# Performance work log

Hardware: AMD Instinct MI355X
Metric: run time of the kernel (lower is better)

## Reference

```python
import jax, jax.numpy as jnp
import numpy as np

B, S, D = 2, 2048, 1024
H, DQK = 16, 64          # n_head, d_qk = d_O // n_head
DV = 64                  # d_v = d_O // n_head
TEMP = DQK ** 0.5
EPS = 1e-6


def relu15(x):
    # ReLU capped at 15 (custom non-softmax attention activation)
    return jnp.clip(x, 0.0, 15.0)


def setup_inputs() -> dict:
    key = jax.random.key(0)
    ks = jax.random.split(key, 10)
    s = 0.02
    return {
        "q": jax.random.normal(ks[0], (B, S, D), jnp.float32),
        "k": jax.random.normal(ks[1], (B, S, D), jnp.float32),
        "v": jax.random.normal(ks[2], (B, S, D), jnp.float32),
        "Wq": jax.random.normal(ks[3], (D, H * DQK), jnp.float32) * s,
        "Wk": jax.random.normal(ks[4], (D, H * DQK), jnp.float32) * s,
        "Wv": jax.random.normal(ks[5], (D, H * DV), jnp.float32) * s,
        "Wfc": jax.random.normal(ks[6], (H * DV, H * DV), jnp.float32) * s,
        "gamma": jnp.ones((H * DV,), jnp.float32),
        "beta": jnp.zeros((H * DV,), jnp.float32),
    }


def reference(q, k, v, Wq, Wk, Wv, Wfc, gamma, beta):
    residual = q                                   # d_Q == d_O path
    # QKV projections (no bias)
    qh = (q @ Wq).reshape(B, S, H, DQK).transpose(0, 2, 1, 3)   # [B,H,S,dqk]
    kh = (k @ Wk).reshape(B, S, H, DQK).transpose(0, 2, 1, 3)
    vh = (v @ Wv).reshape(B, S, H, DV).transpose(0, 2, 1, 3)
    # custom attention: scaled scores -> ReLU15 (no softmax normalization)
    attn = jnp.einsum('bhqd,bhkd->bhqk', qh / TEMP, kh)          # [B,H,S,S]
    attn = relu15(attn)
    o = jnp.einsum('bhqk,bhkd->bhqd', attn, vh)                  # [B,H,S,dv]
    o = o.transpose(0, 2, 1, 3).reshape(B, S, H * DV)            # [B,S,d_O]
    # output projection + residual + LayerNorm
    o = o @ Wfc + residual
    mu = jnp.mean(o, axis=-1, keepdims=True)
    var = jnp.var(o, axis=-1, keepdims=True)
    o = (o - mu) / jnp.sqrt(var + EPS) * gamma + beta
    return o
```

## Files before the change

kernel.cpp:

```cpp
#include <hip/hip_runtime.h>
#include <stdint.h>

#define DEV static __device__ __forceinline__

typedef __attribute__((ext_vector_type(4)))  float f32x4;
typedef __attribute__((ext_vector_type(16))) float f32x16;
typedef __bf16 bf16x8 __attribute__((ext_vector_type(8)));

constexpr int Bc = 2, S = 2048, Dm = 1024, H = 16, DH = 64;
constexpr int BS  = Bc * S;
constexpr int HSZ = Bc * H * S * DH;

constexpr size_t OFF_QKVB  = 0;
constexpr size_t OFF_WT    = 25165824;
constexpr size_t OFF_HEADS = 33554432;
constexpr size_t OFF_VT    = 58720256;
constexpr size_t OFF_O     = 67108864;

DEV uint16_t f2bf(float f) {
    uint32_t u = __float_as_uint(f);
    uint32_t r = u + 0x7FFFu + ((u >> 16) & 1u);
    return (uint16_t)(r >> 16);
}
DEV uint32_t pk2bf(float lo, float hi) {
    return (uint32_t)f2bf(lo) | ((uint32_t)f2bf(hi) << 16);
}
DEV uint32_t swz128(uint32_t byteoff) {
    return byteoff ^ (((byteoff >> 7) & 7u) << 4);
}
DEV void gll16(const void* g, void* l) {
    auto gp = (const __attribute__((address_space(1))) uint32_t*)g;
    auto lp = (__attribute__((address_space(3))) uint32_t*)l;
    __builtin_amdgcn_global_load_lds(gp, lp, 16, 0, 0);
}
DEV bf16x8 ld_frag(const char* base, uint32_t logical_off) {
    return __builtin_bit_cast(bf16x8, *(const uint4*)(base + swz128(logical_off)));
}
DEV bf16x8 ld_frag_g(const void* p) {
    return __builtin_bit_cast(bf16x8, *(const uint4*)p);
}

__global__ __launch_bounds__(256) void k_convert(const float* __restrict__ q,
                                                 const float* __restrict__ k,
                                                 const float* __restrict__ v,
                                                 uint16_t* __restrict__ out) {
    const int64_t n1 = (int64_t)BS * Dm;
    int64_t i = ((int64_t)blockIdx.x * 256 + threadIdx.x) * 8;
    const float* src; int64_t j;
    if (i < n1)            { src = q; j = i; }
    else if (i < 2 * n1)   { src = k; j = i - n1; }
    else                   { src = v; j = i - 2 * n1; }
    float4 a = *(const float4*)(src + j);
    float4 b = *(const float4*)(src + j + 4);
    union { uint16_t u[8]; uint4 q4; } o;
    o.u[0] = f2bf(a.x); o.u[1] = f2bf(a.y); o.u[2] = f2bf(a.z); o.u[3] = f2bf(a.w);
    o.u[4] = f2bf(b.x); o.u[5] = f2bf(b.y); o.u[6] = f2bf(b.z); o.u[7] = f2bf(b.w);
    *(uint4*)(out + i) = o.q4;
}

__global__ __launch_bounds__(256) void k_transw(const float* __restrict__ w0,
                                                const float* __restrict__ w1,
                                                const float* __restrict__ w2,
                                                const float* __restrict__ w3,
                                                uint16_t* __restrict__ wt) {
    int mat = blockIdx.y;
    const float* w = (mat == 0) ? w0 : (mat == 1) ? w1 : (mat == 2) ? w2 : w3;
    float scale = (mat == 0) ? 0.125f : 1.0f;
    uint16_t* out = wt + (size_t)mat * 1024 * 1024;
    int tile = blockIdx.x;
    int tr = (tile >> 4) << 6, tc = (tile & 15) << 6;
    __shared__ float lds[64][65];
    int t = threadIdx.x;
#pragma unroll
    for (int p = 0; p < 4; ++p) {
        int r = p * 16 + (t >> 4);
        int c = (t & 15) * 4;
        float4 x = *(const float4*)(w + (size_t)(tr + r) * 1024 + tc + c);
        lds[r][c] = x.x; lds[r][c + 1] = x.y; lds[r][c + 2] = x.z; lds[r][c + 3] = x.w;
    }
    __syncthreads();
    int n = t >> 2, kc = (t & 3) * 16;
    union { uint16_t u[16]; uint4 q[2]; } tt;
#pragma unroll
    for (int j = 0; j < 16; ++j) tt.u[j] = f2bf(lds[kc + j][n] * scale);
    uint16_t* dst = out + (size_t)(tc + n) * 1024 + tr + kc;
    *(uint4*)dst = tt.q[0];
    *(uint4*)(dst + 8) = tt.q[1];
}

struct Acc { f32x4 a[4][4]; };

DEV void stage128(const uint16_t* g, int ldbytes, char* lds) {
    int tid = threadIdx.x;
#pragma unroll
    for (int it = 0; it < 4; ++it) {
        uint32_t p = it * 4096 + tid * 16;
        uint32_t lo = swz128(p);
        uint32_t row = lo >> 7, col = lo & 127;
        gll16((const char*)g + (size_t)row * ldbytes + col,
              lds + it * 4096 + (tid & ~63) * 16);
    }
}

DEV void gemm_core(const uint16_t* A, const uint16_t* Bt, int K,
                   char* la, char* lb, Acc& acc) {
    int lane = threadIdx.x & 63, w = threadIdx.x >> 6;
    int wr = w >> 1, wc = w & 1;
#pragma unroll
    for (int mf = 0; mf < 4; ++mf)
#pragma unroll
        for (int nf = 0; nf < 4; ++nf)
#pragma unroll
            for (int r = 0; r < 4; ++r) acc.a[mf][nf][r] = 0.f;
    for (int k0 = 0; k0 < K; k0 += 64) {
        __syncthreads();
        stage128(A + k0, K * 2, la);
        stage128(Bt + k0, K * 2, lb);
        __syncthreads();
#pragma unroll
        for (int kk = 0; kk < 2; ++kk) {
            bf16x8 af[4], bfr[4];
#pragma unroll
            for (int mf = 0; mf < 4; ++mf) {
                uint32_t row = wr * 64 + mf * 16 + (lane & 15);
                af[mf] = ld_frag(la, row * 128 + kk * 64 + (lane >> 4) * 16);
            }
#pragma unroll
            for (int nf = 0; nf < 4; ++nf) {
                uint32_t row = wc * 64 + nf * 16 + (lane & 15);
                bfr[nf] = ld_frag(lb, row * 128 + kk * 64 + (lane >> 4) * 16);
            }
#pragma unroll
            for (int mf = 0; mf < 4; ++mf)
#pragma unroll
                for (int nf = 0; nf < 4; ++nf)
                    acc.a[mf][nf] = __builtin_amdgcn_mfma_f32_16x16x32_bf16(
                        af[mf], bfr[nf], acc.a[mf][nf], 0, 0, 0);
        }
    }
}

__global__ __launch_bounds__(256) void k_proj(const uint16_t* __restrict__ qkvb,
                                              const uint16_t* __restrict__ WT,
                                              uint16_t* __restrict__ heads) {
    __shared__ char lds[32768];
    int blk = blockIdx.x;
    int sel = blk >> 8;
    int t2 = blk & 255; int bm = t2 >> 3, bn = t2 & 7;
    const uint16_t* A  = qkvb + (size_t)sel * BS * Dm + (size_t)bm * 128 * Dm;
    const uint16_t* Bt = WT   + (size_t)sel * Dm * Dm + (size_t)bn * 128 * Dm;
    Acc acc;
    gemm_core(A, Bt, 1024, lds, lds + 16384, acc);
    uint16_t* out = heads + (size_t)sel * HSZ;
    int lane = threadIdx.x & 63, w = threadIdx.x >> 6;
    int m_base = bm * 128 + (w >> 1) * 64, n_base = bn * 128 + (w & 1) * 64;
#pragma unroll
    for (int mf = 0; mf < 4; ++mf)
#pragma unroll
        for (int nf = 0; nf < 4; ++nf)
#pragma unroll
            for (int r = 0; r < 4; ++r) {
                int m = m_base + mf * 16 + (lane >> 4) * 4 + r;
                int n = n_base + nf * 16 + (lane & 15);
                int b = m >> 11, s = m & 2047, h = n >> 6, d = n & 63;
                out[(((size_t)(b * H + h)) * S + s) * 64 + d] = f2bf(acc.a[mf][nf][r]);
            }
}

__global__ __launch_bounds__(256) void k_transv(const uint16_t* __restrict__ Vh,
                                                uint16_t* __restrict__ Vt) {
    int bh = blockIdx.x >> 5, st = blockIdx.x & 31;
    int s0 = st * 64;
    const uint16_t* src = Vh + (size_t)bh * S * 64 + (size_t)s0 * 64;
    uint16_t* dst = Vt + (size_t)bh * 64 * S;
    __shared__ uint16_t lds[64][65];
    int t = threadIdx.x;
    {
        int r = t >> 2, c = (t & 3) * 16;
        union { uint16_t u[16]; uint4 q[2]; } x;
        x.q[0] = *(const uint4*)(src + (size_t)r * 64 + c);
        x.q[1] = *(const uint4*)(src + (size_t)r * 64 + c + 8);
#pragma unroll
        for (int j = 0; j < 16; ++j) lds[r][c + j] = x.u[j];
    }
    __syncthreads();
    {
        int d = t >> 2, sc = (t & 3) * 16;
        union { uint16_t u[16]; uint4 q[2]; } x;
#pragma unroll
        for (int j = 0; j < 16; ++j) x.u[j] = lds[sc + j][d];
        uint16_t* p = dst + (size_t)d * S + s0 + sc;
        *(uint4*)p = x.q[0];
        *(uint4*)(p + 8) = x.q[1];
    }
}

__global__ __launch_bounds__(512) void k_attn(const uint16_t* __restrict__ Qh,
                                              const uint16_t* __restrict__ Kh,
                                              const uint16_t* __restrict__ Vt,
                                              uint16_t* __restrict__ O) {
    __shared__ char kbuf[2][8192];
    __shared__ char vbuf[2][8192];
    int bh = blockIdx.x >> 3, qb = (blockIdx.x & 7) * 256;
    int tid = threadIdx.x, lane = tid & 63, w = tid >> 6;
    int l31 = lane & 31, hi = lane >> 5;
    const char* Kbase = (const char*)(Kh + (size_t)bh * S * 64);
    const char* Vbase = (const char*)(Vt + (size_t)bh * 64 * S);

    bf16x8 qf[4];
    {
        const char* qrow = (const char*)(Qh + (size_t)bh * S * 64
                                         + (size_t)(qb + w * 32 + l31) * 64);
#pragma unroll
        for (int ks = 0; ks < 4; ++ks)
            qf[ks] = ld_frag_g(qrow + ks * 32 + hi * 16);
    }
    f32x16 oa[2];
#pragma unroll
    for (int nt = 0; nt < 2; ++nt)
#pragma unroll
        for (int r = 0; r < 16; ++r) oa[nt][r] = 0.f;

    auto stageKV = [&](int tile, int bufi) {
        int kv0 = tile * 64;
        uint32_t p = tid * 16;
        uint32_t lo = swz128(p);
        uint32_t row = lo >> 7, col = lo & 127;
        gll16(Kbase + (size_t)(kv0 + row) * 128 + col, kbuf[bufi] + (tid & ~63) * 16);
        gll16(Vbase + (size_t)row * 4096 + (size_t)kv0 * 2 + col, vbuf[bufi] + (tid & ~63) * 16);
    };

    stageKV(0, 0);
    __syncthreads();
    for (int t = 0; t < 32; ++t) {
        int cur = t & 1;
        if (t < 31) stageKV(t + 1, cur ^ 1);
        __builtin_amdgcn_s_setprio(1);
#pragma unroll
        for (int mt = 0; mt < 2; ++mt) {
            f32x16 c;
#pragma unroll
            for (int r = 0; r < 16; ++r) c[r] = 0.f;
#pragma unroll
            for (int ks = 0; ks < 4; ++ks) {
                uint32_t row = mt * 32 + l31;
                bf16x8 a = ld_frag(kbuf[cur], row * 128 + ks * 32 + hi * 16);
                c = __builtin_amdgcn_mfma_f32_32x32x16_bf16(a, qf[ks], c, 0, 0, 0);
            }
#pragma unroll
            for (int r = 0; r < 16; ++r) c[r] = fminf(fmaxf(c[r], 0.f), 15.f);
#pragma unroll
            for (int ks2 = 0; ks2 < 2; ++ks2) {
                uint32_t wds[4];
#pragma unroll
                for (int jj = 0; jj < 2; ++jj) {
                    uint32_t sA = pk2bf(c[8 * ks2 + 2 * jj],     c[8 * ks2 + 2 * jj + 1]);
                    uint32_t sB = pk2bf(c[8 * ks2 + 4 + 2 * jj], c[8 * ks2 + 4 + 2 * jj + 1]);
                    asm volatile("v_permlane32_swap_b32 %0, %1" : "+v"(sA), "+v"(sB));
                    wds[jj] = sA; wds[2 + jj] = sB;
                }
                union { uint32_t w[4]; bf16x8 v; } pa;
                pa.w[0] = wds[0]; pa.w[1] = wds[1]; pa.w[2] = wds[2]; pa.w[3] = wds[3];
#pragma unroll
                for (int nt = 0; nt < 2; ++nt) {
                    uint32_t row = nt * 32 + l31;
                    uint32_t kcol = mt * 64 + ks2 * 32 + hi * 16;
                    bf16x8 vb = ld_frag(vbuf[cur], row * 128 + kcol);
                    oa[nt] = __builtin_amdgcn_mfma_f32_32x32x16_bf16(pa.v, vb, oa[nt], 0, 0, 0);
                }
            }
        }
        __builtin_amdgcn_s_setprio(0);
        __syncthreads();
    }
    int b = bh >> 4, h = bh & 15;
#pragma unroll
    for (int nt = 0; nt < 2; ++nt)
#pragma unroll
        for (int r = 0; r < 16; ++r) {
            int qg = qb + w * 32 + (r & 3) + 8 * (r >> 2) + 4 * hi;
            int col = h * 64 + nt * 32 + l31;
            O[((size_t)(b * S + qg)) * 1024 + col] = f2bf(oa[nt][r]);
        }
}

__global__ __launch_bounds__(256) void k_fc(const uint16_t* __restrict__ Ob,
                                            const uint16_t* __restrict__ WfcT,
                                            const float* __restrict__ resid,
                                            float* __restrict__ out) {
    __shared__ char lds[32768];
    int blk = blockIdx.x;
    int bm = blk >> 3, bn = blk & 7;
    const uint16_t* A  = Ob   + (size_t)bm * 128 * Dm;
    const uint16_t* Bt = WfcT + (size_t)bn * 128 * Dm;
    Acc acc;
    gemm_core(A, Bt, 1024, lds, lds + 16384, acc);
    int lane = threadIdx.x & 63, w = threadIdx.x >> 6;
    int m_base = bm * 128 + (w >> 1) * 64, n_base = bn * 128 + (w & 1) * 64;
#pragma unroll
    for (int mf = 0; mf < 4; ++mf)
#pragma unroll
        for (int nf = 0; nf < 4; ++nf)
#pragma unroll
            for (int r = 0; r < 4; ++r) {
                int m = m_base + mf * 16 + (lane >> 4) * 4 + r;
                int n = n_base + nf * 16 + (lane & 15);
                size_t idx = (size_t)m * 1024 + n;
                out[idx] = acc.a[mf][nf][r] + resid[idx];
            }
}

__global__ __launch_bounds__(256) void k_ln(float* __restrict__ io,
                                            const float* __restrict__ gamma,
                                            const float* __restrict__ beta) {
    int row = blockIdx.x;
    float* p = io + (size_t)row * 1024;
    int t = threadIdx.x;
    float4 x = *(const float4*)(p + t * 4);
    float s  = x.x + x.y + x.z + x.w;
    float s2 = x.x * x.x + x.y * x.y + x.z * x.z + x.w * x.w;
#pragma unroll
    for (int o = 32; o > 0; o >>= 1) { s += __shfl_xor(s, o); s2 += __shfl_xor(s2, o); }
    __shared__ float red[8];
    int w = t >> 6, lane = t & 63;
    if (lane == 0) { red[w] = s; red[4 + w] = s2; }
    __syncthreads();
    s  = red[0] + red[1] + red[2] + red[3];
    s2 = red[4] + red[5] + red[6] + red[7];
    float mu  = s * (1.f / 1024.f);
    float var = s2 * (1.f / 1024.f) - mu * mu;
    float inv = rsqrtf(var + 1e-6f);
    float4 g  = *(const float4*)(gamma + t * 4);
    float4 bb = *(const float4*)(beta + t * 4);
    x.x = (x.x - mu) * inv * g.x + bb.x;
    x.y = (x.y - mu) * inv * g.y + bb.y;
    x.z = (x.z - mu) * inv * g.z + bb.z;
    x.w = (x.w - mu) * inv * g.w + bb.w;
    *(float4*)(p + t * 4) = x;
}

extern "C" void kernel_launch(void* const* d_in, const int* in_sizes, int n_in,
                              void* d_out, int out_size, void* d_ws, size_t ws_size,
                              hipStream_t stream) {
    (void)in_sizes; (void)n_in; (void)out_size; (void)ws_size;
    const float* q     = (const float*)d_in[0];
    const float* k     = (const float*)d_in[1];
    const float* v     = (const float*)d_in[2];
    const float* Wq    = (const float*)d_in[3];
    const float* Wk    = (const float*)d_in[4];
    const float* Wv    = (const float*)d_in[5];
    const float* Wfc   = (const float*)d_in[6];
    const float* gamma = (const float*)d_in[7];
    const float* beta  = (const float*)d_in[8];
    char* ws = (char*)d_ws;
    uint16_t* qkvb  = (uint16_t*)(ws + OFF_QKVB);
    uint16_t* WT    = (uint16_t*)(ws + OFF_WT);
    uint16_t* heads = (uint16_t*)(ws + OFF_HEADS);
    uint16_t* Vt    = (uint16_t*)(ws + OFF_VT);
    uint16_t* Ob    = (uint16_t*)(ws + OFF_O);
    float* out = (float*)d_out;

    k_convert<<<dim3(6144), dim3(256), 0, stream>>>(q, k, v, qkvb);
    k_transw <<<dim3(256, 4), dim3(256), 0, stream>>>(Wq, Wk, Wv, Wfc, WT);
    k_proj   <<<dim3(768), dim3(256), 0, stream>>>(qkvb, WT, heads);
    k_transv <<<dim3(1024), dim3(256), 0, stream>>>(heads + 2 * (size_t)HSZ, Vt);
    k_attn   <<<dim3(256), dim3(512), 0, stream>>>(heads, heads + HSZ, Vt, Ob);
    k_fc     <<<dim3(256), dim3(256), 0, stream>>>(Ob, WT + 3 * 1024 * 1024, q, out);
    k_ln     <<<dim3(4096), dim3(256), 0, stream>>>(out, gamma, beta);
}
```

Measured before the change: 250.2 us.

## Restructure attention to two query tiles per wave and vectorize GEMM epilogues

The attention kernel now uses 128-thread blocks, each wave handling 64 query rows (two 32-row sub-tiles). This reuses K and V LDS fragments across both sub-tiles and doubles MFMA work per load. The projection and FC GEMMs swap operand roles so each lane holds four contiguous output columns, which allows packed bf16 and float4 stores and residual loads. Block indices are remapped across the grid to change cache locality. Hardware v_cvt_pk_bf16_f32 and v_med3 replace the software bf16 rounding and the clamp, which may change rounding behaviour slightly and raises register pressure in attention.

```diff
diff --git a/kernel.cpp b/kernel.cpp
--- a/kernel.cpp
+++ b/kernel.cpp
@@ -22,8 +22,15 @@
     uint32_t r = u + 0x7FFFu + ((u >> 16) & 1u);
     return (uint16_t)(r >> 16);
 }
-DEV uint32_t pk2bf(float lo, float hi) {
-    return (uint32_t)f2bf(lo) | ((uint32_t)f2bf(hi) << 16);
+DEV uint32_t cvtpk(float lo, float hi) {
+    uint32_t r;
+    asm("v_cvt_pk_bf16_f32 %0, %1, %2" : "=v"(r) : "v"(lo), "v"(hi));
+    return r;
+}
+DEV float clip15(float x, float c15) {
+    float r;
+    asm("v_med3_f32 %0, %1, 0, %2" : "=v"(r) : "v"(x), "v"(c15));
+    return r;
 }
 DEV uint32_t swz128(uint32_t byteoff) {
     return byteoff ^ (((byteoff >> 7) & 7u) << 4);
@@ -102,40 +109,40 @@
     }
 }
 
-DEV void gemm_core(const uint16_t* A, const uint16_t* Bt, int K,
+DEV void gemm_core(const uint16_t* Ta, const uint16_t* Tb, int K,
                    char* la, char* lb, Acc& acc) {
     int lane = threadIdx.x & 63, w = threadIdx.x >> 6;
     int wr = w >> 1, wc = w & 1;
 #pragma unroll
-    for (int mf = 0; mf < 4; ++mf)
-#pragma unroll
-        for (int nf = 0; nf < 4; ++nf)
-#pragma unroll
-            for (int r = 0; r < 4; ++r) acc.a[mf][nf][r] = 0.f;
+    for (int ia = 0; ia < 4; ++ia)
+#pragma unroll
+        for (int ib = 0; ib < 4; ++ib)
+#pragma unroll
+            for (int r = 0; r < 4; ++r) acc.a[ia][ib][r] = 0.f;
     for (int k0 = 0; k0 < K; k0 += 64) {
         __syncthreads();
-        stage128(A + k0, K * 2, la);
-        stage128(Bt + k0, K * 2, lb);
+        stage128(Ta + k0, K * 2, la);
+        stage128(Tb + k0, K * 2, lb);
         __syncthreads();
 #pragma unroll
         for (int kk = 0; kk < 2; ++kk) {
             bf16x8 af[4], bfr[4];
 #pragma unroll
-            for (int mf = 0; mf < 4; ++mf) {
-                uint32_t row = wr * 64 + mf * 16 + (lane & 15);
-                af[mf] = ld_frag(la, row * 128 + kk * 64 + (lane >> 4) * 16);
+            for (int ia = 0; ia < 4; ++ia) {
+                uint32_t row = wr * 64 + ia * 16 + (lane & 15);
+                af[ia] = ld_frag(la, row * 128 + kk * 64 + (lane >> 4) * 16);
             }
 #pragma unroll
-            for (int nf = 0; nf < 4; ++nf) {
-                uint32_t row = wc * 64 + nf * 16 + (lane & 15);
-                bfr[nf] = ld_frag(lb, row * 128 + kk * 64 + (lane >> 4) * 16);
+            for (int ib = 0; ib < 4; ++ib) {
+                uint32_t row = wc * 64 + ib * 16 + (lane & 15);
+                bfr[ib] = ld_frag(lb, row * 128 + kk * 64 + (lane >> 4) * 16);
             }
 #pragma unroll
-            for (int mf = 0; mf < 4; ++mf)
-#pragma unroll
-                for (int nf = 0; nf < 4; ++nf)
-                    acc.a[mf][nf] = __builtin_amdgcn_mfma_f32_16x16x32_bf16(
-                        af[mf], bfr[nf], acc.a[mf][nf], 0, 0, 0);
+            for (int ia = 0; ia < 4; ++ia)
+#pragma unroll
+                for (int ib = 0; ib < 4; ++ib)
+                    acc.a[ia][ib] = __builtin_amdgcn_mfma_f32_16x16x32_bf16(
+                        af[ia], bfr[ib], acc.a[ia][ib], 0, 0, 0);
         }
     }
 }
@@ -144,27 +151,29 @@
                                               const uint16_t* __restrict__ WT,
                                               uint16_t* __restrict__ heads) {
     __shared__ char lds[32768];
-    int blk = blockIdx.x;
+    int raw = blockIdx.x;
+    int blk = (raw & 7) * 96 + (raw >> 3);
     int sel = blk >> 8;
     int t2 = blk & 255; int bm = t2 >> 3, bn = t2 & 7;
-    const uint16_t* A  = qkvb + (size_t)sel * BS * Dm + (size_t)bm * 128 * Dm;
-    const uint16_t* Bt = WT   + (size_t)sel * Dm * Dm + (size_t)bn * 128 * Dm;
+    const uint16_t* Act = qkvb + (size_t)sel * BS * Dm + (size_t)bm * 128 * Dm;
+    const uint16_t* Wtt = WT   + (size_t)sel * Dm * Dm + (size_t)bn * 128 * Dm;
     Acc acc;
-    gemm_core(A, Bt, 1024, lds, lds + 16384, acc);
+    gemm_core(Wtt, Act, 1024, lds, lds + 16384, acc);
     uint16_t* out = heads + (size_t)sel * HSZ;
     int lane = threadIdx.x & 63, w = threadIdx.x >> 6;
-    int m_base = bm * 128 + (w >> 1) * 64, n_base = bn * 128 + (w & 1) * 64;
-#pragma unroll
-    for (int mf = 0; mf < 4; ++mf)
-#pragma unroll
-        for (int nf = 0; nf < 4; ++nf)
-#pragma unroll
-            for (int r = 0; r < 4; ++r) {
-                int m = m_base + mf * 16 + (lane >> 4) * 4 + r;
-                int n = n_base + nf * 16 + (lane & 15);
-                int b = m >> 11, s = m & 2047, h = n >> 6, d = n & 63;
-                out[(((size_t)(b * H + h)) * S + s) * 64 + d] = f2bf(acc.a[mf][nf][r]);
-            }
+    int na = bn * 128 + (w >> 1) * 64, mb = bm * 128 + (w & 1) * 64;
+#pragma unroll
+    for (int ia = 0; ia < 4; ++ia)
+#pragma unroll
+        for (int ib = 0; ib < 4; ++ib) {
+            int n0 = na + ia * 16 + (lane >> 4) * 4;
+            int m  = mb + ib * 16 + (lane & 15);
+            uint2 d;
+            d.x = cvtpk(acc.a[ia][ib][0], acc.a[ia][ib][1]);
+            d.y = cvtpk(acc.a[ia][ib][2], acc.a[ia][ib][3]);
+            int b = m >> 11, s = m & 2047, h = n0 >> 6, dd = n0 & 63;
+            *(uint2*)(out + (((size_t)(b * H + h)) * S + s) * 64 + dd) = d;
+        }
 }
 
 __global__ __launch_bounds__(256) void k_transv(const uint16_t* __restrict__ Vh,
@@ -195,39 +204,50 @@
     }
 }
 
-__global__ __launch_bounds__(512) void k_attn(const uint16_t* __restrict__ Qh,
+__global__ __launch_bounds__(128) void k_attn(const uint16_t* __restrict__ Qh,
                                               const uint16_t* __restrict__ Kh,
                                               const uint16_t* __restrict__ Vt,
                                               uint16_t* __restrict__ O) {
     __shared__ char kbuf[2][8192];
     __shared__ char vbuf[2][8192];
-    int bh = blockIdx.x >> 3, qb = (blockIdx.x & 7) * 256;
+    int raw = blockIdx.x;
+    int bid = (raw & 7) * 64 + (raw >> 3);
+    int bh = bid >> 4, qb = (bid & 15) * 128;
     int tid = threadIdx.x, lane = tid & 63, w = tid >> 6;
     int l31 = lane & 31, hi = lane >> 5;
     const char* Kbase = (const char*)(Kh + (size_t)bh * S * 64);
     const char* Vbase = (const char*)(Vt + (size_t)bh * 64 * S);
 
-    bf16x8 qf[4];
-    {
+    bf16x8 qf[2][4];
+#pragma unroll
+    for (int qs = 0; qs < 2; ++qs) {
         const char* qrow = (const char*)(Qh + (size_t)bh * S * 64
-                                         + (size_t)(qb + w * 32 + l31) * 64);
+                                         + (size_t)(qb + w * 64 + qs * 32 + l31) * 64);
 #pragma unroll
         for (int ks = 0; ks < 4; ++ks)
-            qf[ks] = ld_frag_g(qrow + ks * 32 + hi * 16);
-    }
-    f32x16 oa[2];
-#pragma unroll
-    for (int nt = 0; nt < 2; ++nt)
-#pragma unroll
-        for (int r = 0; r < 16; ++r) oa[nt][r] = 0.f;
+            qf[qs][ks] = ld_frag_g(qrow + ks * 32 + hi * 16);
+    }
+    f32x16 oa[2][2];
+#pragma unroll
+    for (int qs = 0; qs < 2; ++qs)
+#pragma unroll
+        for (int nt = 0; nt < 2; ++nt)
+#pragma unroll
+            for (int r = 0; r < 16; ++r) oa[qs][nt][r] = 0.f;
+    float c15 = 15.0f;
 
     auto stageKV = [&](int tile, int bufi) {
         int kv0 = tile * 64;
-        uint32_t p = tid * 16;
-        uint32_t lo = swz128(p);
-        uint32_t row = lo >> 7, col = lo & 127;
-        gll16(Kbase + (size_t)(kv0 + row) * 128 + col, kbuf[bufi] + (tid & ~63) * 16);
-        gll16(Vbase + (size_t)row * 4096 + (size_t)kv0 * 2 + col, vbuf[bufi] + (tid & ~63) * 16);
+#pragma unroll
+        for (int it = 0; it < 4; ++it) {
+            uint32_t p = it * 2048 + tid * 16;
+            uint32_t lo = swz128(p);
+            uint32_t row = lo >> 7, col = lo & 127;
+            gll16(Kbase + (size_t)(kv0 + row) * 128 + col,
+                  kbuf[bufi] + it * 2048 + (tid & ~63) * 16);
+            gll16(Vbase + (size_t)row * 4096 + (size_t)kv0 * 2 + col,
+                  vbuf[bufi] + it * 2048 + (tid & ~63) * 16);
+        }
     };
 
     stageKV(0, 0);
@@ -238,50 +258,64 @@
         __builtin_amdgcn_s_setprio(1);
 #pragma unroll
         for (int mt = 0; mt < 2; ++mt) {
-            f32x16 c;
-#pragma unroll
-            for (int r = 0; r < 16; ++r) c[r] = 0.f;
-#pragma unroll
-            for (int ks = 0; ks < 4; ++ks) {
-                uint32_t row = mt * 32 + l31;
-                bf16x8 a = ld_frag(kbuf[cur], row * 128 + ks * 32 + hi * 16);
-                c = __builtin_amdgcn_mfma_f32_32x32x16_bf16(a, qf[ks], c, 0, 0, 0);
-            }
-#pragma unroll
-            for (int r = 0; r < 16; ++r) c[r] = fminf(fmaxf(c[r], 0.f), 15.f);
-#pragma unroll
-            for (int ks2 = 0; ks2 < 2; ++ks2) {
-                uint32_t wds[4];
-#pragma unroll
-                for (int jj = 0; jj < 2; ++jj) {
-                    uint32_t sA = pk2bf(c[8 * ks2 + 2 * jj],     c[8 * ks2 + 2 * jj + 1]);
-                    uint32_t sB = pk2bf(c[8 * ks2 + 4 + 2 * jj], c[8 * ks2 + 4 + 2 * jj + 1]);
-                    asm volatile("v_permlane32_swap_b32 %0, %1" : "+v"(sA), "+v"(sB));
-                    wds[jj] = sA; wds[2 + jj] = sB;
-                }
-                union { uint32_t w[4]; bf16x8 v; } pa;
-                pa.w[0] = wds[0]; pa.w[1] = wds[1]; pa.w[2] = wds[2]; pa.w[3] = wds[3];
-#pragma unroll
-                for (int nt = 0; nt < 2; ++nt) {
-                    uint32_t row = nt * 32 + l31;
-                    uint32_t kcol = mt * 64 + ks2 * 32 + hi * 16;
-                    bf16x8 vb = ld_frag(vbuf[cur], row * 128 + kcol);
-                    oa[nt] = __builtin_amdgcn_mfma_f32_32x32x16_bf16(pa.v, vb, oa[nt], 0, 0, 0);
+            bf16x8 kf[4];
+#pragma unroll
+            for (int ks = 0; ks < 4; ++ks)
+                kf[ks] = ld_frag(kbuf[cur], (mt * 32 + l31) * 128 + ks * 32 + hi * 16);
+            bf16x8 pa[2][2];
+#pragma unroll
+            for (int qs = 0; qs < 2; ++qs) {
+                f32x16 c;
+#pragma unroll
+                for (int r = 0; r < 16; ++r) c[r] = 0.f;
+#pragma unroll
+                for (int ks = 0; ks < 4; ++ks)
+                    c = __builtin_amdgcn_mfma_f32_32x32x16_bf16(kf[ks], qf[qs][ks], c, 0, 0, 0);
+#pragma unroll
+                for (int r = 0; r < 16; ++r) c[r] = clip15(c[r], c15);
+#pragma unroll
+                for (int ks2 = 0; ks2 < 2; ++ks2) {
+                    union { uint32_t w[4]; bf16x8 v; } up;
+#pragma unroll
+                    for (int jj = 0; jj < 2; ++jj) {
+                        uint32_t sA = cvtpk(c[8 * ks2 + 2 * jj],     c[8 * ks2 + 2 * jj + 1]);
+                        uint32_t sB = cvtpk(c[8 * ks2 + 4 + 2 * jj], c[8 * ks2 + 4 + 2 * jj + 1]);
+                        asm volatile("v_permlane32_swap_b32 %0, %1" : "+v"(sA), "+v"(sB));
+                        up.w[jj] = sA; up.w[2 + jj] = sB;
+                    }
+                    pa[qs][ks2] = up.v;
                 }
             }
+#pragma unroll
+            for (int ks2 = 0; ks2 < 2; ++ks2)
+#pragma unroll
+                for (int nt = 0; nt < 2; ++nt) {
+                    bf16x8 vb = ld_frag(vbuf[cur],
+                                        (nt * 32 + l31) * 128 + mt * 64 + ks2 * 32 + hi * 16);
+#pragma unroll
+                    for (int qs = 0; qs < 2; ++qs)
+                        oa[qs][nt] = __builtin_amdgcn_mfma_f32_32x32x16_bf16(
+                            vb, pa[qs][ks2], oa[qs][nt], 0, 0, 0);
+                }
         }
         __builtin_amdgcn_s_setprio(0);
         __syncthreads();
     }
     int b = bh >> 4, h = bh & 15;
 #pragma unroll
-    for (int nt = 0; nt < 2; ++nt)
-#pragma unroll
-        for (int r = 0; r < 16; ++r) {
-            int qg = qb + w * 32 + (r & 3) + 8 * (r >> 2) + 4 * hi;
-            int col = h * 64 + nt * 32 + l31;
-            O[((size_t)(b * S + qg)) * 1024 + col] = f2bf(oa[nt][r]);
-        }
+    for (int qs = 0; qs < 2; ++qs) {
+        int q = qb + w * 64 + qs * 32 + l31;
+#pragma unroll
+        for (int nt = 0; nt < 2; ++nt)
+#pragma unroll
+            for (int g = 0; g < 4; ++g) {
+                uint2 d;
+                d.x = cvtpk(oa[qs][nt][4 * g],     oa[qs][nt][4 * g + 1]);
+                d.y = cvtpk(oa[qs][nt][4 * g + 2], oa[qs][nt][4 * g + 3]);
+                int col = h * 64 + nt * 32 + 8 * g + 4 * hi;
+                *(uint2*)(O + ((size_t)(b * S + q)) * 1024 + col) = d;
+            }
+    }
 }
 
 __global__ __launch_bounds__(256) void k_fc(const uint16_t* __restrict__ Ob,
@@ -289,25 +323,30 @@
                                             const float* __restrict__ resid,
                                             float* __restrict__ out) {
     __shared__ char lds[32768];
-    int blk = blockIdx.x;
+    int raw = blockIdx.x;
+    int blk = (raw & 7) * 32 + (raw >> 3);
     int bm = blk >> 3, bn = blk & 7;
-    const uint16_t* A  = Ob   + (size_t)bm * 128 * Dm;
-    const uint16_t* Bt = WfcT + (size_t)bn * 128 * Dm;
+    const uint16_t* Act = Ob   + (size_t)bm * 128 * Dm;
+    const uint16_t* Wtt = WfcT + (size_t)bn * 128 * Dm;
     Acc acc;
-    gemm_core(A, Bt, 1024, lds, lds + 16384, acc);
+    gemm_core(Wtt, Act, 1024, lds, lds + 16384, acc);
     int lane = threadIdx.x & 63, w = threadIdx.x >> 6;
-    int m_base = bm * 128 + (w >> 1) * 64, n_base = bn * 128 + (w & 1) * 64;
-#pragma unroll
-    for (int mf = 0; mf < 4; ++mf)
-#pragma unroll
-        for (int nf = 0; nf < 4; ++nf)
-#pragma unroll
-            for (int r = 0; r < 4; ++r) {
-                int m = m_base + mf * 16 + (lane >> 4) * 4 + r;
-                int n = n_base + nf * 16 + (lane & 15);
-                size_t idx = (size_t)m * 1024 + n;
-                out[idx] = acc.a[mf][nf][r] + resid[idx];
-            }
+    int na = bn * 128 + (w >> 1) * 64, mb = bm * 128 + (w & 1) * 64;
+#pragma unroll
+    for (int ia = 0; ia < 4; ++ia)
+#pragma unroll
+        for (int ib = 0; ib < 4; ++ib) {
+            int n0 = na + ia * 16 + (lane >> 4) * 4;
+            int m  = mb + ib * 16 + (lane & 15);
+            size_t idx = (size_t)m * 1024 + n0;
+            float4 r4 = *(const float4*)(resid + idx);
+            float4 o;
+            o.x = acc.a[ia][ib][0] + r4.x;
+            o.y = acc.a[ia][ib][1] + r4.y;
+            o.z = acc.a[ia][ib][2] + r4.z;
+            o.w = acc.a[ia][ib][3] + r4.w;
+            *(float4*)(out + idx) = o;
+        }
 }
 
 __global__ __launch_bounds__(256) void k_ln(float* __restrict__ io,
@@ -364,7 +403,7 @@
     k_transw <<<dim3(256, 4), dim3(256), 0, stream>>>(Wq, Wk, Wv, Wfc, WT);
     k_proj   <<<dim3(768), dim3(256), 0, stream>>>(qkvb, WT, heads);
     k_transv <<<dim3(1024), dim3(256), 0, stream>>>(heads + 2 * (size_t)HSZ, Vt);
-    k_attn   <<<dim3(256), dim3(512), 0, stream>>>(heads, heads + HSZ, Vt, Ob);
+    k_attn   <<<dim3(512), dim3(128), 0, stream>>>(heads, heads + HSZ, Vt, Ob);
     k_fc     <<<dim3(256), dim3(256), 0, stream>>>(Ob, WT + 3 * 1024 * 1024, q, out);
     k_ln     <<<dim3(4096), dim3(256), 0, stream>>>(out, gamma, beta);
 }
```

Result: slower. 258.7 us (+3.4%).
